# Kernel tuning notes

Hardware: AMD Instinct MI355X
Metric: run time of the kernel (lower is better)

## Reference

```python
import jax, jax.numpy as jnp
import numpy as np

B, T, HID = 4, 2048, 2048
H, DK, DV = 16, 128, 128
EPS = 1e-5


def setup_inputs() -> dict:
    key = jax.random.key(0)
    ks = jax.random.split(key, 14)
    w = lambda k, shape, s=0.02: jax.random.normal(k, shape, jnp.float32) * s
    return dict(
        hidden_states=jax.random.normal(ks[0], (B, T, HID), jnp.float32),
        recurrent_state=jnp.zeros((B, H, DK, DV), jnp.float32),
        q_w=w(ks[1], (H * DK, HID)),
        k_w=w(ks[2], (H * DK, HID)),
        v_w=w(ks[3], (H * DV, HID)),
        f_w0=w(ks[4], (DV, HID)),
        f_w1=w(ks[5], (H * DK, DV)),
        b_w=w(ks[6], (H, HID)),
        A_log=jnp.log(jax.random.uniform(ks[7], (H,), jnp.float32, 1.0, 16.0)),
        dt_bias=w(ks[8], (H * DK,), 0.1),
        g_w0=w(ks[9], (DV, HID)),
        g_w1=w(ks[10], (H * DV, DV)),
        g_b1=w(ks[11], (H * DV,), 0.1),
        o_norm_weight=jnp.ones((DV,), jnp.float32),
        o_w=w(ks[12], (HID, H * DV)),
    )


def _l2norm(x):
    return x * jax.lax.rsqrt(jnp.sum(x * x, -1, keepdims=True) + 1e-6)


def _kda_scan(q, k, v, g, beta, S0):
    # time-major inputs: q,k,g [T,B,H,DK]; v [T,B,H,DV]; beta [T,B,H]; S0 [B,H,DK,DV]
    scale = DK ** -0.5

    def step(S, inp):
        qt, kt, vt, gt, bt = inp
        S = S * jnp.exp(gt)[..., None]                      # per-key-dim decay
        kv = jnp.einsum('bhk,bhkv->bhv', kt, S)             # current readout for k
        delta = (vt - kv) * bt[..., None]                   # beta-weighted correction
        S = S + kt[..., :, None] * delta[..., None, :]      # rank-1 delta update
        ot = jnp.einsum('bhk,bhkv->bhv', qt * scale, S)
        return S, ot

    S, o = jax.lax.scan(step, S0, (q, k, v, g, beta))
    return o, S


def reference(hidden_states, recurrent_state, q_w, k_w, v_w, f_w0, f_w1, b_w,
              A_log, dt_bias, g_w0, g_w1, g_b1, o_norm_weight, o_w):
    h = hidden_states
    q = jax.nn.silu(h @ q_w.T).reshape(B, T, H, DK)
    k = jax.nn.silu(h @ k_w.T).reshape(B, T, H, DK)
    v = jax.nn.silu(h @ v_w.T).reshape(B, T, H, DV)
    # fused_kda_gate: g = -exp(A_log) * softplus(g + dt_bias), per key channel
    g = ((h @ f_w0.T) @ f_w1.T).reshape(B, T, H, DK)
    g = -jnp.exp(A_log)[None, None, :, None] * jax.nn.softplus(g + dt_bias.reshape(H, DK))
    beta = jax.nn.sigmoid(h @ b_w.T)  # [B,T,H]
    q = _l2norm(q)
    k = _l2norm(k)
    tm = lambda x: jnp.swapaxes(x, 0, 1)  # -> time-major
    o, S = _kda_scan(tm(q), tm(k), tm(v), tm(g), tm(beta), recurrent_state)
    o = jnp.swapaxes(o, 0, 1)  # [B,T,H,DV]
    factor = ((h @ g_w0.T) @ g_w1.T + g_b1).reshape(B, T, H, DV)
    # FusedRMSNormGated(activation='sigmoid'): rmsnorm then sigmoid gate
    o = o * jax.lax.rsqrt(jnp.mean(o * o, -1, keepdims=True) + EPS)
    o = o * o_norm_weight * jax.nn.sigmoid(factor)
    out = o.reshape(B, T, H * DV) @ o_w.T
    return out, S
```

## Files before the change

kernel.cpp:

```cpp
#include <hip/hip_runtime.h>
#include <math.h>


typedef short short8 __attribute__((ext_vector_type(8)));
typedef float f32x4 __attribute__((ext_vector_type(4)));
typedef unsigned short ushort_t;

enum { M_PLAIN = 0, M_QKV = 1, M_LOWRANK = 2, M_GATE = 3, M_FACTOR = 4 };

__device__ __forceinline__ unsigned short f32_to_bf16(float f) {
  unsigned int u = __float_as_uint(f);
  u += 0x7FFFu + ((u >> 16) & 1u);
  return (unsigned short)(u >> 16);
}

__device__ __forceinline__ float silu(float x) { return x / (1.f + __expf(-x)); }

__device__ __forceinline__ void gld_lds16(const void* g, void* l) {
  __builtin_amdgcn_global_load_lds(
      (const __attribute__((address_space(1))) unsigned int*)g,
      (__attribute__((address_space(3))) unsigned int*)l, 16, 0, 0);
}

__device__ __forceinline__ float row16_sum(float x) {
  x += __int_as_float(__builtin_amdgcn_update_dpp(0, __float_as_int(x), 0xB1, 0xF, 0xF, true));
  x += __int_as_float(__builtin_amdgcn_update_dpp(0, __float_as_int(x), 0x4E, 0xF, 0xF, true));
  x += __int_as_float(__builtin_amdgcn_update_dpp(0, __float_as_int(x), 0x141, 0xF, 0xF, true));
  x += __int_as_float(__builtin_amdgcn_update_dpp(0, __float_as_int(x), 0x140, 0xF, 0xF, true));
  return x;
}

__global__ __launch_bounds__(256) void gemm_bf16(
    const ushort_t* __restrict__ A, const ushort_t* __restrict__ W,
    int M, int N, int K, int mode,
    float* __restrict__ f0, float* __restrict__ f1, float* __restrict__ f2,
    ushort_t* __restrict__ b0, ushort_t* __restrict__ b1,
    const float* __restrict__ bias, const float* __restrict__ A_log,
    const float* __restrict__ dt_bias) {
  __shared__ alignas(16) ushort_t As[4096];
  __shared__ alignas(16) ushort_t Bs[4096];
  __shared__ float l2s[2][128];
  const int tid = threadIdx.x;
  const int wv = tid >> 6, ln = tid & 63;
  const int bm = blockIdx.y * 128, bn = blockIdx.x * 128;
  const int wm = wv >> 1, wn = wv & 1;

  const int srow = tid >> 2;
  const int skg = (tid & 3) ^ ((srow >> 1) & 3);
  const size_t ag0 = (size_t)(bm + srow) * K + skg * 8;
  const size_t ag1 = ag0 + (size_t)64 * K;
  const size_t bg0 = (size_t)(bn + srow) * K + skg * 8;
  const size_t bg1 = bg0 + (size_t)64 * K;
  char* const lA = (char*)As;
  char* const lB = (char*)Bs;
  const int wbase = wv * 1024;

  const int fr = ln & 15, fq = ln >> 4;
  const int pg = fq ^ ((fr >> 1) & 3);
  int aoff[4], boff[4];
#pragma unroll
  for (int i = 0; i < 4; i++) {
    aoff[i] = (wm * 64 + i * 16 + fr) * 64 + pg * 16;
    boff[i] = (wn * 64 + i * 16 + fr) * 64 + pg * 16;
  }

  f32x4 acc[4][4];
#pragma unroll
  for (int i = 0; i < 4; i++)
#pragma unroll
    for (int j = 0; j < 4; j++) {
      acc[i][j][0] = 0.f; acc[i][j][1] = 0.f; acc[i][j][2] = 0.f; acc[i][j][3] = 0.f;
    }

  for (int k0 = 0; k0 < K; k0 += 32) {
    gld_lds16(A + ag0 + k0, lA + wbase);
    gld_lds16(A + ag1 + k0, lA + 4096 + wbase);
    gld_lds16(W + bg0 + k0, lB + wbase);
    gld_lds16(W + bg1 + k0, lB + 4096 + wbase);
    __syncthreads();
    short8 af[4], bf[4];
#pragma unroll
    for (int i = 0; i < 4; i++) af[i] = *(const short8*)(lA + aoff[i]);
#pragma unroll
    for (int i = 0; i < 4; i++) bf[i] = *(const short8*)(lB + boff[i]);
#pragma unroll
    for (int i = 0; i < 4; i++)
#pragma unroll
      for (int j = 0; j < 4; j++)
        acc[i][j] = __builtin_amdgcn_mfma_f32_16x16x32_bf16(af[i], bf[j], acc[i][j], 0, 0, 0);
    __syncthreads();
  }

  const int cc = ln & 15, cq = ln >> 4;

  if (mode == M_QKV) {
#pragma unroll
    for (int i = 0; i < 4; i++)
#pragma unroll
      for (int j = 0; j < 4; j++)
#pragma unroll
        for (int r = 0; r < 4; r++) acc[i][j][r] = silu(acc[i][j][r]);
    const bool isqk = (bn < 4096);
    float invr[4][4];
    if (isqk) {
      const float scale = (bn < 2048) ? 0.08838834764831845f : 1.0f;
#pragma unroll
      for (int i = 0; i < 4; i++)
#pragma unroll
        for (int r = 0; r < 4; r++) {
          float ss = 0.f;
#pragma unroll
          for (int j = 0; j < 4; j++) ss = fmaf(acc[i][j][r], acc[i][j][r], ss);
          ss = row16_sum(ss);
          if (cc == 0) l2s[wn][wm * 64 + i * 16 + cq * 4 + r] = ss;
        }
      __syncthreads();
#pragma unroll
      for (int i = 0; i < 4; i++)
#pragma unroll
        for (int r = 0; r < 4; r++) {
          const int rl = wm * 64 + i * 16 + cq * 4 + r;
          invr[i][r] = rsqrtf(l2s[0][rl] + l2s[1][rl] + 1e-6f) * scale;
        }
    } else {
#pragma unroll
      for (int i = 0; i < 4; i++)
#pragma unroll
        for (int r = 0; r < 4; r++) invr[i][r] = 1.f;
    }
    float* dst = (bn < 2048) ? f0 : ((bn < 4096) ? f1 : f2);
    const int nb = bn & 2047;
#pragma unroll
    for (int i = 0; i < 4; i++)
#pragma unroll
      for (int r = 0; r < 4; r++) {
        const int gm = bm + wm * 64 + i * 16 + cq * 4 + r;
#pragma unroll
        for (int j = 0; j < 4; j++) {
          const int gn = nb + wn * 64 + j * 16 + cc;
          dst[(size_t)gm * 2048 + gn] = acc[i][j][r] * invr[i][r];
        }
      }
    return;
  }

  if (mode == M_LOWRANK) {
#pragma unroll
    for (int i = 0; i < 4; i++)
#pragma unroll
      for (int r = 0; r < 4; r++) {
        const int gm = bm + wm * 64 + i * 16 + cq * 4 + r;
#pragma unroll
        for (int j = 0; j < 4; j++) {
          const int gn = bn + wn * 64 + j * 16 + cc;
          const float x = acc[i][j][r];
          if (gn < 128) b0[(size_t)gm * 128 + gn] = f32_to_bf16(x);
          else if (gn < 256) b1[(size_t)gm * 128 + (gn - 128)] = f32_to_bf16(x);
          else if (gn < 272) f0[(size_t)gm * 16 + (gn - 256)] = 1.f / (1.f + __expf(-x));
        }
      }
    return;
  }

#pragma unroll
  for (int i = 0; i < 4; i++)
#pragma unroll
    for (int r = 0; r < 4; r++) {
      const int gm = bm + wm * 64 + i * 16 + cq * 4 + r;
#pragma unroll
      for (int j = 0; j < 4; j++) {
        const int gn = bn + wn * 64 + j * 16 + cc;
        float x = acc[i][j][r];
        if (mode == M_FACTOR) x += bias[gn];
        else if (mode == M_GATE) {
          const float y = x + dt_bias[gn];
          const float sp = fmaxf(y, 0.f) + log1pf(__expf(-fabsf(y)));
          x = __expf(-__expf(A_log[gn >> 7]) * sp);
        }
        f0[(size_t)gm * N + gn] = x;
      }
    }
}

__global__ __launch_bounds__(256) void cast_bf16(const float* __restrict__ x,
                                                 ushort_t* __restrict__ y, int n) {
  const int i = (blockIdx.x * 256 + threadIdx.x) * 4;
  if (i >= n) return;
  const float4 v = *(const float4*)&x[i];
  union { ushort_t u[4]; uint2 v2; } o;
  o.u[0] = f32_to_bf16(v.x); o.u[1] = f32_to_bf16(v.y);
  o.u[2] = f32_to_bf16(v.z); o.u[3] = f32_to_bf16(v.w);
  *(uint2*)&y[i] = o.v2;
}

__global__ __launch_bounds__(64, 2) void kda_scan(
    const float* __restrict__ q, const float* __restrict__ k,
    const float* __restrict__ v, const float* __restrict__ ge,
    const float* __restrict__ beta, const float* __restrict__ S0,
    float* __restrict__ o, float* __restrict__ S_out) {
  const int bid = blockIdx.x;
  const int bh = (((bid >> 3) & 7) << 3) | (bid & 7);
  const int cg = bid >> 6;
  const int h = bh & 15, b = bh >> 4;
  const int ln = threadIdx.x;
  const int cl = ln >> 4, kg = ln & 15;
  const int col = cg * 4 + cl;
  const int kof = kg * 8;

  __shared__ alignas(16) char lds[12288];

  const size_t s_base = (size_t)bh * (128 * 128);
  const size_t rb = (size_t)b * (2048 * 2048) + (size_t)h * 128;
  const size_t bbase = (size_t)(b * 2048) * 16 + h;

  const char* kc = (const char*)(k + rb);
  const char* qc = (const char*)(q + rb);
  const char* gc = (const char*)(ge + rb);
  const float* vbp  = v + rb;
  const float* vbp2 = vbp + 2048;
  const float* bbp  = beta + bbase;
  const float* bbp2 = bbp + 16;
  float* obp  = o + rb;
  float* obp2 = obp + 2048;
  const float* S0b = S0 + s_base;

  const int cpos = ln & 31;
  const int gch = (cpos & ~1) | ((cpos & 1) ^ ((cpos >> 3) & 1));
  const unsigned lane_src = (unsigned)((ln >> 5) * 8192 + gch * 16);

  const unsigned rd0 = (unsigned)(kg * 32 + ((0 ^ ((kg >> 2) & 1)) * 16));
  const unsigned rd1 = (unsigned)(kg * 32 + ((1 ^ ((kg >> 2) & 1)) * 16));

  const unsigned voff_v = (unsigned)(col * 4);
  const unsigned voff_b = 0u;
  const unsigned voff_o = (unsigned)(col * 4);

  float S[8];
#pragma unroll
  for (int j = 0; j < 8; ++j) {
    const unsigned offs = (unsigned)(((kof + j) * 128 + col) * 4);
    asm volatile("global_load_dword %0, %1, %2" : "=v"(S[j]) : "v"(offs), "s"(S0b));
  }

  float Vs[8], Bs[8], Os[8];
  f32x4 K0a, K1a, Q0a, Q1a, G0a, G1a;
  f32x4 K0b, K1b, Q0b, Q1b, G0b, G1b;

#define WAITV(N) do { asm volatile("s_waitcnt vmcnt(" #N ")" ::: "memory"); \
                      __builtin_amdgcn_sched_barrier(0); } while (0)
#define WAITL(N) do { asm volatile("s_waitcnt lgkmcnt(" #N ")" ::: "memory"); \
                      __builtin_amdgcn_sched_barrier(0); } while (0)
#define DSR(dst, a, IMM) \
  asm volatile("ds_read_b128 %0, %1 offset:%c2" : "=v"(dst) : "v"(a), "n"(IMM))

#define READS(SFX, SL, PH)                                    \
  do {                                                        \
    DSR(K0##SFX, rd0, ((SL)*3 + 0) * 1024 + (PH)*512);        \
    DSR(K1##SFX, rd1, ((SL)*3 + 0) * 1024 + (PH)*512);        \
    DSR(Q0##SFX, rd0, ((SL)*3 + 1) * 1024 + (PH)*512);        \
    DSR(Q1##SFX, rd1, ((SL)*3 + 1) * 1024 + (PH)*512);        \
    DSR(G0##SFX, rd0, ((SL)*3 + 2) * 1024 + (PH)*512);        \
    DSR(G1##SFX, rd1, ((SL)*3 + 2) * 1024 + (PH)*512);        \
  } while (0)

#define STAGE(SL)                                                                                    \
  do {                                                                                               \
    gld_lds16(kc + lane_src, lds + ((SL)*3 + 0) * 1024); kc += 16384;                                \
    gld_lds16(qc + lane_src, lds + ((SL)*3 + 1) * 1024); qc += 16384;                                \
    gld_lds16(gc + lane_src, lds + ((SL)*3 + 2) * 1024); gc += 16384;                                \
    asm volatile("global_load_dword %0, %1, %2" : "=v"(Vs[2*(SL)])   : "v"(voff_v), "s"(vbp));       \
    asm volatile("global_load_dword %0, %1, %2" : "=v"(Vs[2*(SL)+1]) : "v"(voff_v), "s"(vbp2));      \
    vbp += 4096; vbp2 += 4096;                                                                       \
    asm volatile("global_load_dword %0, %1, %2" : "=v"(Bs[2*(SL)])   : "v"(voff_b), "s"(bbp));       \
    asm volatile("global_load_dword %0, %1, %2" : "=v"(Bs[2*(SL)+1]) : "v"(voff_b), "s"(bbp2));      \
    bbp += 32; bbp2 += 32;                                                                           \
  } while (0)

#define STORES(U)                                                                                    \
  do {                                                                                               \
    if (kg == 0) {                                                                                   \
      asm volatile("global_store_dword %0, %1, %2" :: "v"(voff_o), "v"(Os[(U)-1]), "s"(obp) : "memory");  \
      asm volatile("global_store_dword %0, %1, %2" :: "v"(voff_o), "v"(Os[(U)]), "s"(obp2) : "memory");   \
    }                                                                                                \
    obp += 4096; obp2 += 4096;                                                                       \
  } while (0)

#define COMPUTE(SFX, U)                                                                              \
  do {                                                                                               \
    float p0 = 0.f, p1 = 0.f, o0 = 0.f, o1 = 0.f, d0 = 0.f, d1 = 0.f;                                \
    S[0] *= G0##SFX[0]; p0 = fmaf(K0##SFX[0], S[0], p0); o0 = fmaf(Q0##SFX[0], S[0], o0); d0 = fmaf(Q0##SFX[0], K0##SFX[0], d0); \
    S[1] *= G0##SFX[1]; p1 = fmaf(K0##SFX[1], S[1], p1); o1 = fmaf(Q0##SFX[1], S[1], o1); d1 = fmaf(Q0##SFX[1], K0##SFX[1], d1); \
    S[2] *= G0##SFX[2]; p0 = fmaf(K0##SFX[2], S[2], p0); o0 = fmaf(Q0##SFX[2], S[2], o0); d0 = fmaf(Q0##SFX[2], K0##SFX[2], d0); \
    S[3] *= G0##SFX[3]; p1 = fmaf(K0##SFX[3], S[3], p1); o1 = fmaf(Q0##SFX[3], S[3], o1); d1 = fmaf(Q0##SFX[3], K0##SFX[3], d1); \
    S[4] *= G1##SFX[0]; p0 = fmaf(K1##SFX[0], S[4], p0); o0 = fmaf(Q1##SFX[0], S[4], o0); d0 = fmaf(Q1##SFX[0], K1##SFX[0], d0); \
    S[5] *= G1##SFX[1]; p1 = fmaf(K1##SFX[1], S[5], p1); o1 = fmaf(Q1##SFX[1], S[5], o1); d1 = fmaf(Q1##SFX[1], K1##SFX[1], d1); \
    S[6] *= G1##SFX[2]; p0 = fmaf(K1##SFX[2], S[6], p0); o0 = fmaf(Q1##SFX[2], S[6], o0); d0 = fmaf(Q1##SFX[2], K1##SFX[2], d0); \
    S[7] *= G1##SFX[3]; p1 = fmaf(K1##SFX[3], S[7], p1); o1 = fmaf(Q1##SFX[3], S[7], o1); d1 = fmaf(Q1##SFX[3], K1##SFX[3], d1); \
    const float p  = row16_sum(p0 + p1);                                                             \
    const float oq = row16_sum(o0 + o1);                                                             \
    const float qk = row16_sum(d0 + d1);                                                             \
    const float delta = (Vs[(U)] - p) * Bs[(U)];                                                     \
    Os[(U)] = fmaf(qk, delta, oq);                                                                   \
    S[0] = fmaf(K0##SFX[0], delta, S[0]);                                                            \
    S[1] = fmaf(K0##SFX[1], delta, S[1]);                                                            \
    S[2] = fmaf(K0##SFX[2], delta, S[2]);                                                            \
    S[3] = fmaf(K0##SFX[3], delta, S[3]);                                                            \
    S[4] = fmaf(K1##SFX[0], delta, S[4]);                                                            \
    S[5] = fmaf(K1##SFX[1], delta, S[5]);                                                            \
    S[6] = fmaf(K1##SFX[2], delta, S[6]);                                                            \
    S[7] = fmaf(K1##SFX[3], delta, S[7]);                                                            \
  } while (0)

#define STEP_EVEN(U, SL) \
  do { READS(b, SL, 1); WAITL(6); COMPUTE(a, U); } while (0)
#define STEP_ODD(U, SL, NSL, WV) \
  do { WAITV(WV); READS(a, NSL, 0); WAITL(6); COMPUTE(b, U); STAGE(SL); STORES(U); } while (0)

#define ITER(W1, W3, W5, W7)                          \
  do {                                                \
    STEP_EVEN(0, 0);                                  \
    STEP_ODD(1, 0, 1, W1);                            \
    STEP_EVEN(2, 1);                                  \
    STEP_ODD(3, 1, 2, W3);                            \
    STEP_EVEN(4, 2);                                  \
    STEP_ODD(5, 2, 3, W5);                            \
    STEP_EVEN(6, 3);                                  \
    STEP_ODD(7, 3, 0, W7);                            \
  } while (0)

  STAGE(0);
  STAGE(1);
  STAGE(2);
  STAGE(3);
  WAITV(21);
  READS(a, 0, 0);

  ITER(14, 16, 18, 20);
  for (int it = 1; it < 256; ++it) {
    ITER(20, 20, 20, 20);
  }

  WAITL(0);
  WAITV(0);

#pragma unroll
  for (int j = 0; j < 8; ++j)
    S_out[s_base + (size_t)(kof + j) * 128 + col] = S[j];

#undef ITER
#undef STEP_ODD
#undef STEP_EVEN
#undef COMPUTE
#undef STORES
#undef STAGE
#undef READS
#undef DSR
#undef WAITL
#undef WAITV
}

__global__ __launch_bounds__(256) void gate_rmsnorm(
    const float* __restrict__ o, const float* __restrict__ factor,
    const float* __restrict__ w, ushort_t* __restrict__ out) {
  const int ln = threadIdx.x & 63, wv = threadIdx.x >> 6;
  const float w0 = w[ln * 2], w1 = w[ln * 2 + 1];
  const size_t row0 = (size_t)blockIdx.x * 64 + wv * 16;
  for (int it = 0; it < 16; it++) {
    const size_t base = (row0 + it) * 128 + ln * 2;
    const float2 x = *(const float2*)&o[base];
    const float2 f = *(const float2*)&factor[base];
    float ss = fmaf(x.x, x.x, x.y * x.y);
    ss = row16_sum(ss);
    ss += __shfl_xor(ss, 16);
    ss += __shfl_xor(ss, 32);
    const float r = rsqrtf(ss * (1.f / 128.f) + 1e-5f);
    const float y0 = x.x * r * w0 / (1.f + __expf(-f.x));
    const float y1 = x.y * r * w1 / (1.f + __expf(-f.y));
    *(unsigned int*)&out[base] =
        (unsigned int)f32_to_bf16(y0) | ((unsigned int)f32_to_bf16(y1) << 16);
  }
}

extern "C" void kernel_launch(void* const* d_in, const int* in_sizes, int n_in,
                              void* d_out, int out_size, void* d_ws, size_t ws_size,
                              hipStream_t stream) {
  const float* h    = (const float*)d_in[0];
  const float* S0   = (const float*)d_in[1];
  const float* q_w  = (const float*)d_in[2];
  const float* k_w  = (const float*)d_in[3];
  const float* v_w  = (const float*)d_in[4];
  const float* f_w0 = (const float*)d_in[5];
  const float* f_w1 = (const float*)d_in[6];
  const float* b_w  = (const float*)d_in[7];
  const float* A_log  = (const float*)d_in[8];
  const float* dt_b   = (const float*)d_in[9];
  const float* g_w0 = (const float*)d_in[10];
  const float* g_w1 = (const float*)d_in[11];
  const float* g_b1 = (const float*)d_in[12];
  const float* o_nw = (const float*)d_in[13];
  const float* o_w  = (const float*)d_in[14];

  float* outp = (float*)d_out;
  float* Sout = outp + (size_t)8192 * 2048;

  const size_t BIG = (size_t)8192 * 2048;
  float* ws = (float*)d_ws;
  float* vbuf  = ws;
  float* qbuf  = vbuf + BIG;
  float* kbuf  = qbuf + BIG;
  float* betab = kbuf + BIG;
  ushort_t* fpreb = (ushort_t*)(betab + (size_t)8192 * 16);
  ushort_t* gpreb = fpreb + (size_t)8192 * 128;
  ushort_t* wf1   = gpreb + (size_t)8192 * 128;
  ushort_t* wg1   = wf1 + (size_t)2048 * 128;
  ushort_t* wo    = wg1 + (size_t)2048 * 128;
  ushort_t* wlow  = wo + (size_t)2048 * 2048;
  ushort_t* hb    = wlow + (size_t)384 * 2048;
  ushort_t* wqkv  = hb + BIG;
  float* obuf = (float*)hb;
  ushort_t* gatedb = (ushort_t*)qbuf;

  const dim3 blk(256);

  cast_bf16<<<16384, blk, 0, stream>>>(h, hb, 8192 * 2048);
  cast_bf16<<<4096, blk, 0, stream>>>(q_w, wqkv, 2048 * 2048);
  cast_bf16<<<4096, blk, 0, stream>>>(k_w, wqkv + (size_t)2048 * 2048, 2048 * 2048);
  cast_bf16<<<4096, blk, 0, stream>>>(v_w, wqkv + (size_t)4096 * 2048, 2048 * 2048);
  cast_bf16<<<4096, blk, 0, stream>>>(o_w, wo, 2048 * 2048);
  cast_bf16<<<256, blk, 0, stream>>>(f_w0, wlow, 128 * 2048);
  cast_bf16<<<256, blk, 0, stream>>>(g_w0, wlow + (size_t)128 * 2048, 128 * 2048);
  cast_bf16<<<32, blk, 0, stream>>>(b_w, wlow + (size_t)256 * 2048, 16 * 2048);
  cast_bf16<<<256, blk, 0, stream>>>(f_w1, wf1, 2048 * 128);
  cast_bf16<<<256, blk, 0, stream>>>(g_w1, wg1, 2048 * 128);

  gemm_bf16<<<dim3(48, 64), blk, 0, stream>>>(hb, wqkv, 8192, 6144, 2048, M_QKV,
      qbuf, kbuf, vbuf, nullptr, nullptr, nullptr, nullptr, nullptr);
  gemm_bf16<<<dim3(3, 64), blk, 0, stream>>>(hb, wlow, 8192, 384, 2048, M_LOWRANK,
      betab, nullptr, nullptr, fpreb, gpreb, nullptr, nullptr, nullptr);
  gemm_bf16<<<dim3(16, 64), blk, 0, stream>>>(fpreb, wf1, 8192, 2048, 128, M_GATE,
      outp, nullptr, nullptr, nullptr, nullptr, nullptr, A_log, dt_b);
  kda_scan<<<2048, 64, 0, stream>>>(qbuf, kbuf, vbuf, outp, betab, S0, obuf, Sout);
  gemm_bf16<<<dim3(16, 64), blk, 0, stream>>>(gpreb, wg1, 8192, 2048, 128, M_FACTOR,
      outp, nullptr, nullptr, nullptr, nullptr, g_b1, nullptr, nullptr);
  gate_rmsnorm<<<2048, blk, 0, stream>>>(obuf, outp, o_nw, gatedb);
  gemm_bf16<<<dim3(16, 64), blk, 0, stream>>>(gatedb, wo, 8192, 2048, 2048, M_PLAIN,
      outp, nullptr, nullptr, nullptr, nullptr, nullptr, nullptr, nullptr);
}
```

Before: 1.828 ms.

## Remap scan lanes to 32 key-groups by 2 value columns with cross-half reduction

Each lane of the KDA scan kernel now holds 4 key rows across 2 value columns, where before it held 8 key rows of 1 column. Wavefront halves split the key dimension and are combined with a permlane32 swap. This cuts the LDS reads per step from six to three and lets V, O and the state move as dwordx2. The cost is a longer reduction chain per dot product (row16 plus a cross-half swap) and five reductions instead of three, on the serial recurrence's critical path.

Measured after the change: 2.061 ms. 12.8% more time.

```diff
diff --git a/kernel.cpp b/kernel.cpp
--- a/kernel.cpp
+++ b/kernel.cpp
@@ -4,6 +4,8 @@
 
 typedef short short8 __attribute__((ext_vector_type(8)));
 typedef float f32x4 __attribute__((ext_vector_type(4)));
+typedef float f32x2 __attribute__((ext_vector_type(2)));
+typedef int int2v __attribute__((ext_vector_type(2)));
 typedef unsigned short ushort_t;
 
 enum { M_PLAIN = 0, M_QKV = 1, M_LOWRANK = 2, M_GATE = 3, M_FACTOR = 4 };
@@ -28,6 +30,13 @@
   x += __int_as_float(__builtin_amdgcn_update_dpp(0, __float_as_int(x), 0x141, 0xF, 0xF, true));
   x += __int_as_float(__builtin_amdgcn_update_dpp(0, __float_as_int(x), 0x140, 0xF, 0xF, true));
   return x;
+}
+
+__device__ __forceinline__ float sum32(float x) {
+  x = row16_sum(x);
+  int2v r = __builtin_amdgcn_permlane32_swap(__float_as_int(x), __float_as_int(x),
+                                             false, false);
+  return __int_as_float(r.x) + __int_as_float(r.y);
 }
 
 __global__ __launch_bounds__(256) void gemm_bf16(
@@ -203,9 +212,10 @@
   const int cg = bid >> 6;
   const int h = bh & 15, b = bh >> 4;
   const int ln = threadIdx.x;
-  const int cl = ln >> 4, kg = ln & 15;
-  const int col = cg * 4 + cl;
-  const int kof = kg * 8;
+  const int cl = (ln >> 4) & 1;
+  const int kg5 = (ln & 15) | (((ln >> 5) & 1) << 4);
+  const int col0 = cg * 4 + cl * 2;
+  const int k0i = kg5 * 4;
 
   __shared__ alignas(16) char lds[12288];
 
@@ -224,27 +234,24 @@
   float* obp2 = obp + 2048;
   const float* S0b = S0 + s_base;
 
-  const int cpos = ln & 31;
-  const int gch = (cpos & ~1) | ((cpos & 1) ^ ((cpos >> 3) & 1));
-  const unsigned lane_src = (unsigned)((ln >> 5) * 8192 + gch * 16);
-
-  const unsigned rd0 = (unsigned)(kg * 32 + ((0 ^ ((kg >> 2) & 1)) * 16));
-  const unsigned rd1 = (unsigned)(kg * 32 + ((1 ^ ((kg >> 2) & 1)) * 16));
-
-  const unsigned voff_v = (unsigned)(col * 4);
+  const unsigned lane_src = (unsigned)((ln >> 5) * 8192 + (ln & 31) * 16);
+  const unsigned rdK = (unsigned)(kg5 * 16);
+
+  const unsigned voff_v = (unsigned)(col0 * 4);
   const unsigned voff_b = 0u;
-  const unsigned voff_o = (unsigned)(col * 4);
-
-  float S[8];
-#pragma unroll
-  for (int j = 0; j < 8; ++j) {
-    const unsigned offs = (unsigned)(((kof + j) * 128 + col) * 4);
-    asm volatile("global_load_dword %0, %1, %2" : "=v"(S[j]) : "v"(offs), "s"(S0b));
-  }
-
-  float Vs[8], Bs[8], Os[8];
-  f32x4 K0a, K1a, Q0a, Q1a, G0a, G1a;
-  f32x4 K0b, K1b, Q0b, Q1b, G0b, G1b;
+  const unsigned voff_o = (unsigned)(col0 * 4);
+
+  f32x2 S2[4];
+#pragma unroll
+  for (int j = 0; j < 4; ++j) {
+    const unsigned offs = (unsigned)(((k0i + j) * 128 + col0) * 4);
+    asm volatile("global_load_dwordx2 %0, %1, %2" : "=v"(S2[j]) : "v"(offs), "s"(S0b));
+  }
+
+  f32x2 Vs2[8], Os2[8];
+  float Bs[8];
+  f32x4 Ka, Qa, Ga;
+  f32x4 Kb, Qb, Gb;
 
 #define WAITV(N) do { asm volatile("s_waitcnt vmcnt(" #N ")" ::: "memory"); \
                       __builtin_amdgcn_sched_barrier(0); } while (0)
@@ -255,12 +262,9 @@
 
 #define READS(SFX, SL, PH)                                    \
   do {                                                        \
-    DSR(K0##SFX, rd0, ((SL)*3 + 0) * 1024 + (PH)*512);        \
-    DSR(K1##SFX, rd1, ((SL)*3 + 0) * 1024 + (PH)*512);        \
-    DSR(Q0##SFX, rd0, ((SL)*3 + 1) * 1024 + (PH)*512);        \
-    DSR(Q1##SFX, rd1, ((SL)*3 + 1) * 1024 + (PH)*512);        \
-    DSR(G0##SFX, rd0, ((SL)*3 + 2) * 1024 + (PH)*512);        \
-    DSR(G1##SFX, rd1, ((SL)*3 + 2) * 1024 + (PH)*512);        \
+    DSR(K##SFX, rdK, ((SL)*3 + 0) * 1024 + (PH)*512);         \
+    DSR(Q##SFX, rdK, ((SL)*3 + 1) * 1024 + (PH)*512);         \
+    DSR(G##SFX, rdK, ((SL)*3 + 2) * 1024 + (PH)*512);         \
   } while (0)
 
 #define STAGE(SL)                                                                                    \
@@ -268,8 +272,8 @@
     gld_lds16(kc + lane_src, lds + ((SL)*3 + 0) * 1024); kc += 16384;                                \
     gld_lds16(qc + lane_src, lds + ((SL)*3 + 1) * 1024); qc += 16384;                                \
     gld_lds16(gc + lane_src, lds + ((SL)*3 + 2) * 1024); gc += 16384;                                \
-    asm volatile("global_load_dword %0, %1, %2" : "=v"(Vs[2*(SL)])   : "v"(voff_v), "s"(vbp));       \
-    asm volatile("global_load_dword %0, %1, %2" : "=v"(Vs[2*(SL)+1]) : "v"(voff_v), "s"(vbp2));      \
+    asm volatile("global_load_dwordx2 %0, %1, %2" : "=v"(Vs2[2*(SL)])   : "v"(voff_v), "s"(vbp));    \
+    asm volatile("global_load_dwordx2 %0, %1, %2" : "=v"(Vs2[2*(SL)+1]) : "v"(voff_v), "s"(vbp2));   \
     vbp += 4096; vbp2 += 4096;                                                                       \
     asm volatile("global_load_dword %0, %1, %2" : "=v"(Bs[2*(SL)])   : "v"(voff_b), "s"(bbp));       \
     asm volatile("global_load_dword %0, %1, %2" : "=v"(Bs[2*(SL)+1]) : "v"(voff_b), "s"(bbp2));      \
@@ -278,43 +282,45 @@
 
 #define STORES(U)                                                                                    \
   do {                                                                                               \
-    if (kg == 0) {                                                                                   \
-      asm volatile("global_store_dword %0, %1, %2" :: "v"(voff_o), "v"(Os[(U)-1]), "s"(obp) : "memory");  \
-      asm volatile("global_store_dword %0, %1, %2" :: "v"(voff_o), "v"(Os[(U)]), "s"(obp2) : "memory");   \
+    if ((ln & 47) == 0) {                                                                            \
+      asm volatile("global_store_dwordx2 %0, %1, %2" :: "v"(voff_o), "v"(Os2[(U)-1]), "s"(obp) : "memory");  \
+      asm volatile("global_store_dwordx2 %0, %1, %2" :: "v"(voff_o), "v"(Os2[(U)]), "s"(obp2) : "memory");   \
     }                                                                                                \
     obp += 4096; obp2 += 4096;                                                                       \
   } while (0)
 
-#define COMPUTE(SFX, U)                                                                              \
+#define COMPUTE(F, U)                                                                                \
   do {                                                                                               \
-    float p0 = 0.f, p1 = 0.f, o0 = 0.f, o1 = 0.f, d0 = 0.f, d1 = 0.f;                                \
-    S[0] *= G0##SFX[0]; p0 = fmaf(K0##SFX[0], S[0], p0); o0 = fmaf(Q0##SFX[0], S[0], o0); d0 = fmaf(Q0##SFX[0], K0##SFX[0], d0); \
-    S[1] *= G0##SFX[1]; p1 = fmaf(K0##SFX[1], S[1], p1); o1 = fmaf(Q0##SFX[1], S[1], o1); d1 = fmaf(Q0##SFX[1], K0##SFX[1], d1); \
-    S[2] *= G0##SFX[2]; p0 = fmaf(K0##SFX[2], S[2], p0); o0 = fmaf(Q0##SFX[2], S[2], o0); d0 = fmaf(Q0##SFX[2], K0##SFX[2], d0); \
-    S[3] *= G0##SFX[3]; p1 = fmaf(K0##SFX[3], S[3], p1); o1 = fmaf(Q0##SFX[3], S[3], o1); d1 = fmaf(Q0##SFX[3], K0##SFX[3], d1); \
-    S[4] *= G1##SFX[0]; p0 = fmaf(K1##SFX[0], S[4], p0); o0 = fmaf(Q1##SFX[0], S[4], o0); d0 = fmaf(Q1##SFX[0], K1##SFX[0], d0); \
-    S[5] *= G1##SFX[1]; p1 = fmaf(K1##SFX[1], S[5], p1); o1 = fmaf(Q1##SFX[1], S[5], o1); d1 = fmaf(Q1##SFX[1], K1##SFX[1], d1); \
-    S[6] *= G1##SFX[2]; p0 = fmaf(K1##SFX[2], S[6], p0); o0 = fmaf(Q1##SFX[2], S[6], o0); d0 = fmaf(Q1##SFX[2], K1##SFX[2], d0); \
-    S[7] *= G1##SFX[3]; p1 = fmaf(K1##SFX[3], S[7], p1); o1 = fmaf(Q1##SFX[3], S[7], o1); d1 = fmaf(Q1##SFX[3], K1##SFX[3], d1); \
-    const float p  = row16_sum(p0 + p1);                                                             \
-    const float oq = row16_sum(o0 + o1);                                                             \
-    const float qk = row16_sum(d0 + d1);                                                             \
-    const float delta = (Vs[(U)] - p) * Bs[(U)];                                                     \
-    Os[(U)] = fmaf(qk, delta, oq);                                                                   \
-    S[0] = fmaf(K0##SFX[0], delta, S[0]);                                                            \
-    S[1] = fmaf(K0##SFX[1], delta, S[1]);                                                            \
-    S[2] = fmaf(K0##SFX[2], delta, S[2]);                                                            \
-    S[3] = fmaf(K0##SFX[3], delta, S[3]);                                                            \
-    S[4] = fmaf(K1##SFX[0], delta, S[4]);                                                            \
-    S[5] = fmaf(K1##SFX[1], delta, S[5]);                                                            \
-    S[6] = fmaf(K1##SFX[2], delta, S[6]);                                                            \
-    S[7] = fmaf(K1##SFX[3], delta, S[7]);                                                            \
+    S2[0] *= G##F[0]; S2[1] *= G##F[1]; S2[2] *= G##F[2]; S2[3] *= G##F[3];                          \
+    float p0 = K##F[0] * S2[0].x;  float p1 = K##F[0] * S2[0].y;                                     \
+    float o0 = Q##F[0] * S2[0].x;  float o1 = Q##F[0] * S2[0].y;                                     \
+    float d  = Q##F[0] * K##F[0];                                                                    \
+    p0 = fmaf(K##F[1], S2[1].x, p0); p1 = fmaf(K##F[1], S2[1].y, p1);                                \
+    o0 = fmaf(Q##F[1], S2[1].x, o0); o1 = fmaf(Q##F[1], S2[1].y, o1);                                \
+    d  = fmaf(Q##F[1], K##F[1], d);                                                                  \
+    p0 = fmaf(K##F[2], S2[2].x, p0); p1 = fmaf(K##F[2], S2[2].y, p1);                                \
+    o0 = fmaf(Q##F[2], S2[2].x, o0); o1 = fmaf(Q##F[2], S2[2].y, o1);                                \
+    d  = fmaf(Q##F[2], K##F[2], d);                                                                  \
+    p0 = fmaf(K##F[3], S2[3].x, p0); p1 = fmaf(K##F[3], S2[3].y, p1);                                \
+    o0 = fmaf(Q##F[3], S2[3].x, o0); o1 = fmaf(Q##F[3], S2[3].y, o1);                                \
+    d  = fmaf(Q##F[3], K##F[3], d);                                                                  \
+    p0 = sum32(p0); p1 = sum32(p1);                                                                  \
+    o0 = sum32(o0); o1 = sum32(o1);                                                                  \
+    d  = sum32(d);                                                                                   \
+    const float dl0 = (Vs2[(U)].x - p0) * Bs[(U)];                                                   \
+    const float dl1 = (Vs2[(U)].y - p1) * Bs[(U)];                                                   \
+    Os2[(U)].x = fmaf(d, dl0, o0);                                                                   \
+    Os2[(U)].y = fmaf(d, dl1, o1);                                                                   \
+    S2[0].x = fmaf(K##F[0], dl0, S2[0].x); S2[0].y = fmaf(K##F[0], dl1, S2[0].y);                    \
+    S2[1].x = fmaf(K##F[1], dl0, S2[1].x); S2[1].y = fmaf(K##F[1], dl1, S2[1].y);                    \
+    S2[2].x = fmaf(K##F[2], dl0, S2[2].x); S2[2].y = fmaf(K##F[2], dl1, S2[2].y);                    \
+    S2[3].x = fmaf(K##F[3], dl0, S2[3].x); S2[3].y = fmaf(K##F[3], dl1, S2[3].y);                    \
   } while (0)
 
 #define STEP_EVEN(U, SL) \
-  do { READS(b, SL, 1); WAITL(6); COMPUTE(a, U); } while (0)
+  do { READS(b, SL, 1); WAITL(3); COMPUTE(a, U); } while (0)
 #define STEP_ODD(U, SL, NSL, WV) \
-  do { WAITV(WV); READS(a, NSL, 0); WAITL(6); COMPUTE(b, U); STAGE(SL); STORES(U); } while (0)
+  do { WAITV(WV); READS(a, NSL, 0); WAITL(3); COMPUTE(b, U); STAGE(SL); STORES(U); } while (0)
 
 #define ITER(W1, W3, W5, W7)                          \
   do {                                                \
@@ -344,8 +350,8 @@
   WAITV(0);
 
 #pragma unroll
-  for (int j = 0; j < 8; ++j)
-    S_out[s_base + (size_t)(kof + j) * 128 + col] = S[j];
+  for (int j = 0; j < 4; ++j)
+    *(f32x2*)&S_out[s_base + (size_t)(k0i + j) * 128 + col0] = S2[j];
 
 #undef ITER
 #undef STEP_ODD
```

## Store q and k in bf16 and restage scan pipeline four timesteps per slot

Applied to the files above, without the earlier changes.

The QKV GEMM epilogue now writes normalized q and k as bf16 instead of fp32, and the recurrent scan kernel reads them as bf16, unpacking them with shifts and masks. The scan's LDS staging is reorganized so each slot holds four timesteps of k/q/g, with wait counts and the V/beta/O load and store patterns adjusted to match. This halves the global and LDS traffic for q and k in the bandwidth- and latency-bound sequential scan. In exchange it adds bf16 rounding error on q and k that feeds a long recurrence, and it makes the hand-tuned wait counts more intricate.

New measurement: 1.742 ms. 1.05x faster.

```diff
diff --git a/kernel.cpp b/kernel.cpp
--- a/kernel.cpp
+++ b/kernel.cpp
@@ -4,6 +4,7 @@
 
 typedef short short8 __attribute__((ext_vector_type(8)));
 typedef float f32x4 __attribute__((ext_vector_type(4)));
+typedef int int4v __attribute__((ext_vector_type(4)));
 typedef unsigned short ushort_t;
 
 enum { M_PLAIN = 0, M_QKV = 1, M_LOWRANK = 2, M_GATE = 3, M_FACTOR = 4 };
@@ -128,7 +129,6 @@
 #pragma unroll
         for (int r = 0; r < 4; r++) invr[i][r] = 1.f;
     }
-    float* dst = (bn < 2048) ? f0 : ((bn < 4096) ? f1 : f2);
     const int nb = bn & 2047;
 #pragma unroll
     for (int i = 0; i < 4; i++)
@@ -138,7 +138,13 @@
 #pragma unroll
         for (int j = 0; j < 4; j++) {
           const int gn = nb + wn * 64 + j * 16 + cc;
-          dst[(size_t)gm * 2048 + gn] = acc[i][j][r] * invr[i][r];
+          const float val = acc[i][j][r] * invr[i][r];
+          if (bn < 4096) {
+            ushort_t* db = (bn < 2048) ? b0 : b1;
+            db[(size_t)gm * 2048 + gn] = f32_to_bf16(val);
+          } else {
+            f2[(size_t)gm * 2048 + gn] = val;
+          }
         }
       }
     return;
@@ -194,7 +200,7 @@
 }
 
 __global__ __launch_bounds__(64, 2) void kda_scan(
-    const float* __restrict__ q, const float* __restrict__ k,
+    const ushort_t* __restrict__ q, const ushort_t* __restrict__ k,
     const float* __restrict__ v, const float* __restrict__ ge,
     const float* __restrict__ beta, const float* __restrict__ S0,
     float* __restrict__ o, float* __restrict__ S_out) {
@@ -207,33 +213,34 @@
   const int col = cg * 4 + cl;
   const int kof = kg * 8;
 
-  __shared__ alignas(16) char lds[12288];
+  __shared__ alignas(16) char lds[16384];
 
   const size_t s_base = (size_t)bh * (128 * 128);
   const size_t rb = (size_t)b * (2048 * 2048) + (size_t)h * 128;
   const size_t bbase = (size_t)(b * 2048) * 16 + h;
 
-  const char* kc = (const char*)(k + rb);
-  const char* qc = (const char*)(q + rb);
-  const char* gc = (const char*)(ge + rb);
-  const float* vbp  = v + rb;
-  const float* vbp2 = vbp + 2048;
-  const float* bbp  = beta + bbase;
-  const float* bbp2 = bbp + 16;
-  float* obp  = o + rb;
-  float* obp2 = obp + 2048;
+  const char* kc = (const char*)k + rb * 2;
+  const char* qc = (const char*)q + rb * 2;
+  const char* gc = (const char*)ge + rb * 4;
+  const float* vbp = v + rb;
+  const float* bbp = beta + bbase;
+  float* obp = o + rb;
   const float* S0b = S0 + s_base;
 
+  const unsigned lane_src_kq = (unsigned)((ln >> 4) * 4096 + (ln & 15) * 16);
   const int cpos = ln & 31;
   const int gch = (cpos & ~1) | ((cpos & 1) ^ ((cpos >> 3) & 1));
-  const unsigned lane_src = (unsigned)((ln >> 5) * 8192 + gch * 16);
-
-  const unsigned rd0 = (unsigned)(kg * 32 + ((0 ^ ((kg >> 2) & 1)) * 16));
-  const unsigned rd1 = (unsigned)(kg * 32 + ((1 ^ ((kg >> 2) & 1)) * 16));
-
-  const unsigned voff_v = (unsigned)(col * 4);
+  const unsigned lane_src_g = (unsigned)((ln >> 5) * 8192 + gch * 16);
+
+  const unsigned rdK = (unsigned)(kg * 16);
+  const unsigned rd0g = (unsigned)(kg * 32 + ((0 ^ ((kg >> 2) & 1)) * 16));
+  const unsigned rd1g = (unsigned)(kg * 32 + ((1 ^ ((kg >> 2) & 1)) * 16));
+
+  const unsigned voff_v0 = (unsigned)(col * 4);
+  const unsigned voff_v1 = voff_v0 + 8192u;
+  const unsigned voff_v2 = voff_v0 + 16384u;
+  const unsigned voff_v3 = voff_v0 + 24576u;
   const unsigned voff_b = 0u;
-  const unsigned voff_o = (unsigned)(col * 4);
 
   float S[8];
 #pragma unroll
@@ -242,9 +249,9 @@
     asm volatile("global_load_dword %0, %1, %2" : "=v"(S[j]) : "v"(offs), "s"(S0b));
   }
 
-  float Vs[8], Bs[8], Os[8];
-  f32x4 K0a, K1a, Q0a, Q1a, G0a, G1a;
-  f32x4 K0b, K1b, Q0b, Q1b, G0b, G1b;
+  float Vs[4][4], Bs[4][4], Os[4];
+  int4v Kda, Qda, Kdb, Qdb;
+  f32x4 G0a, G1a, G0b, G1b;
 
 #define WAITV(N) do { asm volatile("s_waitcnt vmcnt(" #N ")" ::: "memory"); \
                       __builtin_amdgcn_sched_barrier(0); } while (0)
@@ -255,89 +262,103 @@
 
 #define READS(SFX, SL, PH)                                    \
   do {                                                        \
-    DSR(K0##SFX, rd0, ((SL)*3 + 0) * 1024 + (PH)*512);        \
-    DSR(K1##SFX, rd1, ((SL)*3 + 0) * 1024 + (PH)*512);        \
-    DSR(Q0##SFX, rd0, ((SL)*3 + 1) * 1024 + (PH)*512);        \
-    DSR(Q1##SFX, rd1, ((SL)*3 + 1) * 1024 + (PH)*512);        \
-    DSR(G0##SFX, rd0, ((SL)*3 + 2) * 1024 + (PH)*512);        \
-    DSR(G1##SFX, rd1, ((SL)*3 + 2) * 1024 + (PH)*512);        \
-  } while (0)
-
-#define STAGE(SL)                                                                                    \
+    DSR(Kd##SFX, rdK,  (SL)*4096 + (PH)*256);                 \
+    DSR(Qd##SFX, rdK,  (SL)*4096 + 1024 + (PH)*256);          \
+    DSR(G0##SFX, rd0g, (SL)*4096 + 2048 + (PH)*512);          \
+    DSR(G1##SFX, rd1g, (SL)*4096 + 2048 + (PH)*512);          \
+  } while (0)
+
+#define RESTAGE(SL)                                                                                  \
   do {                                                                                               \
-    gld_lds16(kc + lane_src, lds + ((SL)*3 + 0) * 1024); kc += 16384;                                \
-    gld_lds16(qc + lane_src, lds + ((SL)*3 + 1) * 1024); qc += 16384;                                \
-    gld_lds16(gc + lane_src, lds + ((SL)*3 + 2) * 1024); gc += 16384;                                \
-    asm volatile("global_load_dword %0, %1, %2" : "=v"(Vs[2*(SL)])   : "v"(voff_v), "s"(vbp));       \
-    asm volatile("global_load_dword %0, %1, %2" : "=v"(Vs[2*(SL)+1]) : "v"(voff_v), "s"(vbp2));      \
-    vbp += 4096; vbp2 += 4096;                                                                       \
-    asm volatile("global_load_dword %0, %1, %2" : "=v"(Bs[2*(SL)])   : "v"(voff_b), "s"(bbp));       \
-    asm volatile("global_load_dword %0, %1, %2" : "=v"(Bs[2*(SL)+1]) : "v"(voff_b), "s"(bbp2));      \
-    bbp += 32; bbp2 += 32;                                                                           \
-  } while (0)
-
-#define STORES(U)                                                                                    \
+    gld_lds16(kc + lane_src_kq, lds + (SL)*4096);          kc += 16384;                              \
+    gld_lds16(qc + lane_src_kq, lds + (SL)*4096 + 1024);   qc += 16384;                              \
+    gld_lds16(gc + lane_src_g,  lds + (SL)*4096 + 2048);                                             \
+    gld_lds16(gc + 16384 + lane_src_g, lds + (SL)*4096 + 3072); gc += 32768;                         \
+    asm volatile("global_load_dword %0, %1, %2" : "=v"(Vs[SL][0]) : "v"(voff_v0), "s"(vbp));         \
+    asm volatile("global_load_dword %0, %1, %2" : "=v"(Vs[SL][1]) : "v"(voff_v1), "s"(vbp));         \
+    asm volatile("global_load_dword %0, %1, %2" : "=v"(Vs[SL][2]) : "v"(voff_v2), "s"(vbp));         \
+    asm volatile("global_load_dword %0, %1, %2" : "=v"(Vs[SL][3]) : "v"(voff_v3), "s"(vbp));         \
+    vbp += 8192;                                                                                     \
+    asm volatile("global_load_dword %0, %1, %2"            : "=v"(Bs[SL][0]) : "v"(voff_b), "s"(bbp)); \
+    asm volatile("global_load_dword %0, %1, %2 offset:64"  : "=v"(Bs[SL][1]) : "v"(voff_b), "s"(bbp)); \
+    asm volatile("global_load_dword %0, %1, %2 offset:128" : "=v"(Bs[SL][2]) : "v"(voff_b), "s"(bbp)); \
+    asm volatile("global_load_dword %0, %1, %2 offset:192" : "=v"(Bs[SL][3]) : "v"(voff_b), "s"(bbp)); \
+    bbp += 64;                                                                                       \
+  } while (0)
+
+#define STORES(SL)                                                                                   \
   do {                                                                                               \
     if (kg == 0) {                                                                                   \
-      asm volatile("global_store_dword %0, %1, %2" :: "v"(voff_o), "v"(Os[(U)-1]), "s"(obp) : "memory");  \
-      asm volatile("global_store_dword %0, %1, %2" :: "v"(voff_o), "v"(Os[(U)]), "s"(obp2) : "memory");   \
+      asm volatile("global_store_dword %0, %1, %2" :: "v"(voff_v0), "v"(Os[0]), "s"(obp) : "memory"); \
+      asm volatile("global_store_dword %0, %1, %2" :: "v"(voff_v1), "v"(Os[1]), "s"(obp) : "memory"); \
+      asm volatile("global_store_dword %0, %1, %2" :: "v"(voff_v2), "v"(Os[2]), "s"(obp) : "memory"); \
+      asm volatile("global_store_dword %0, %1, %2" :: "v"(voff_v3), "v"(Os[3]), "s"(obp) : "memory"); \
     }                                                                                                \
-    obp += 4096; obp2 += 4096;                                                                       \
-  } while (0)
-
-#define COMPUTE(SFX, U)                                                                              \
+    obp += 8192;                                                                                     \
+  } while (0)
+
+#define COMPUTE(F, SS, U)                                                                            \
   do {                                                                                               \
+    const int4v kd = Kd##F; const int4v qd = Qd##F;                                                  \
+    const float k0 = __int_as_float(kd[0] << 16), k1 = __int_as_float(kd[0] & 0xffff0000);           \
+    const float k2 = __int_as_float(kd[1] << 16), k3 = __int_as_float(kd[1] & 0xffff0000);           \
+    const float k4 = __int_as_float(kd[2] << 16), k5 = __int_as_float(kd[2] & 0xffff0000);           \
+    const float k6 = __int_as_float(kd[3] << 16), k7 = __int_as_float(kd[3] & 0xffff0000);           \
+    const float q0 = __int_as_float(qd[0] << 16), q1 = __int_as_float(qd[0] & 0xffff0000);           \
+    const float q2 = __int_as_float(qd[1] << 16), q3 = __int_as_float(qd[1] & 0xffff0000);           \
+    const float q4 = __int_as_float(qd[2] << 16), q5 = __int_as_float(qd[2] & 0xffff0000);           \
+    const float q6 = __int_as_float(qd[3] << 16), q7 = __int_as_float(qd[3] & 0xffff0000);           \
     float p0 = 0.f, p1 = 0.f, o0 = 0.f, o1 = 0.f, d0 = 0.f, d1 = 0.f;                                \
-    S[0] *= G0##SFX[0]; p0 = fmaf(K0##SFX[0], S[0], p0); o0 = fmaf(Q0##SFX[0], S[0], o0); d0 = fmaf(Q0##SFX[0], K0##SFX[0], d0); \
-    S[1] *= G0##SFX[1]; p1 = fmaf(K0##SFX[1], S[1], p1); o1 = fmaf(Q0##SFX[1], S[1], o1); d1 = fmaf(Q0##SFX[1], K0##SFX[1], d1); \
-    S[2] *= G0##SFX[2]; p0 = fmaf(K0##SFX[2], S[2], p0); o0 = fmaf(Q0##SFX[2], S[2], o0); d0 = fmaf(Q0##SFX[2], K0##SFX[2], d0); \
-    S[3] *= G0##SFX[3]; p1 = fmaf(K0##SFX[3], S[3], p1); o1 = fmaf(Q0##SFX[3], S[3], o1); d1 = fmaf(Q0##SFX[3], K0##SFX[3], d1); \
-    S[4] *= G1##SFX[0]; p0 = fmaf(K1##SFX[0], S[4], p0); o0 = fmaf(Q1##SFX[0], S[4], o0); d0 = fmaf(Q1##SFX[0], K1##SFX[0], d0); \
-    S[5] *= G1##SFX[1]; p1 = fmaf(K1##SFX[1], S[5], p1); o1 = fmaf(Q1##SFX[1], S[5], o1); d1 = fmaf(Q1##SFX[1], K1##SFX[1], d1); \
-    S[6] *= G1##SFX[2]; p0 = fmaf(K1##SFX[2], S[6], p0); o0 = fmaf(Q1##SFX[2], S[6], o0); d0 = fmaf(Q1##SFX[2], K1##SFX[2], d0); \
-    S[7] *= G1##SFX[3]; p1 = fmaf(K1##SFX[3], S[7], p1); o1 = fmaf(Q1##SFX[3], S[7], o1); d1 = fmaf(Q1##SFX[3], K1##SFX[3], d1); \
+    S[0] *= G0##F[0]; p0 = fmaf(k0, S[0], p0); o0 = fmaf(q0, S[0], o0); d0 = fmaf(q0, k0, d0);       \
+    S[1] *= G0##F[1]; p1 = fmaf(k1, S[1], p1); o1 = fmaf(q1, S[1], o1); d1 = fmaf(q1, k1, d1);       \
+    S[2] *= G0##F[2]; p0 = fmaf(k2, S[2], p0); o0 = fmaf(q2, S[2], o0); d0 = fmaf(q2, k2, d0);       \
+    S[3] *= G0##F[3]; p1 = fmaf(k3, S[3], p1); o1 = fmaf(q3, S[3], o1); d1 = fmaf(q3, k3, d1);       \
+    S[4] *= G1##F[0]; p0 = fmaf(k4, S[4], p0); o0 = fmaf(q4, S[4], o0); d0 = fmaf(q4, k4, d0);       \
+    S[5] *= G1##F[1]; p1 = fmaf(k5, S[5], p1); o1 = fmaf(q5, S[5], o1); d1 = fmaf(q5, k5, d1);       \
+    S[6] *= G1##F[2]; p0 = fmaf(k6, S[6], p0); o0 = fmaf(q6, S[6], o0); d0 = fmaf(q6, k6, d0);       \
+    S[7] *= G1##F[3]; p1 = fmaf(k7, S[7], p1); o1 = fmaf(q7, S[7], o1); d1 = fmaf(q7, k7, d1);       \
     const float p  = row16_sum(p0 + p1);                                                             \
     const float oq = row16_sum(o0 + o1);                                                             \
     const float qk = row16_sum(d0 + d1);                                                             \
-    const float delta = (Vs[(U)] - p) * Bs[(U)];                                                     \
-    Os[(U)] = fmaf(qk, delta, oq);                                                                   \
-    S[0] = fmaf(K0##SFX[0], delta, S[0]);                                                            \
-    S[1] = fmaf(K0##SFX[1], delta, S[1]);                                                            \
-    S[2] = fmaf(K0##SFX[2], delta, S[2]);                                                            \
-    S[3] = fmaf(K0##SFX[3], delta, S[3]);                                                            \
-    S[4] = fmaf(K1##SFX[0], delta, S[4]);                                                            \
-    S[5] = fmaf(K1##SFX[1], delta, S[5]);                                                            \
-    S[6] = fmaf(K1##SFX[2], delta, S[6]);                                                            \
-    S[7] = fmaf(K1##SFX[3], delta, S[7]);                                                            \
-  } while (0)
-
-#define STEP_EVEN(U, SL) \
-  do { READS(b, SL, 1); WAITL(6); COMPUTE(a, U); } while (0)
-#define STEP_ODD(U, SL, NSL, WV) \
-  do { WAITV(WV); READS(a, NSL, 0); WAITL(6); COMPUTE(b, U); STAGE(SL); STORES(U); } while (0)
-
-#define ITER(W1, W3, W5, W7)                          \
+    const float delta = (Vs[SS][U] - p) * Bs[SS][U];                                                 \
+    Os[U] = fmaf(qk, delta, oq);                                                                     \
+    S[0] = fmaf(k0, delta, S[0]);                                                                    \
+    S[1] = fmaf(k1, delta, S[1]);                                                                    \
+    S[2] = fmaf(k2, delta, S[2]);                                                                    \
+    S[3] = fmaf(k3, delta, S[3]);                                                                    \
+    S[4] = fmaf(k4, delta, S[4]);                                                                    \
+    S[5] = fmaf(k5, delta, S[5]);                                                                    \
+    S[6] = fmaf(k6, delta, S[6]);                                                                    \
+    S[7] = fmaf(k7, delta, S[7]);                                                                    \
+  } while (0)
+
+#define SLOT(SL, NS, WV)                                           \
+  do {                                                             \
+    READS(b, SL, 1); WAITL(4); COMPUTE(a, SL, 0);                  \
+    READS(a, SL, 2); WAITL(4); COMPUTE(b, SL, 1);                  \
+    READS(b, SL, 3); WAITL(4); COMPUTE(a, SL, 2);                  \
+    WAITV(WV); READS(a, NS, 0); WAITL(4); COMPUTE(b, SL, 3);       \
+    RESTAGE(SL); STORES(SL);                                       \
+  } while (0)
+
+#define ITER(W0, W1, W2, W3)                          \
   do {                                                \
-    STEP_EVEN(0, 0);                                  \
-    STEP_ODD(1, 0, 1, W1);                            \
-    STEP_EVEN(2, 1);                                  \
-    STEP_ODD(3, 1, 2, W3);                            \
-    STEP_EVEN(4, 2);                                  \
-    STEP_ODD(5, 2, 3, W5);                            \
-    STEP_EVEN(6, 3);                                  \
-    STEP_ODD(7, 3, 0, W7);                            \
-  } while (0)
-
-  STAGE(0);
-  STAGE(1);
-  STAGE(2);
-  STAGE(3);
-  WAITV(21);
+    SLOT(0, 1, W0);                                   \
+    SLOT(1, 2, W1);                                   \
+    SLOT(2, 3, W2);                                   \
+    SLOT(3, 0, W3);                                   \
+  } while (0)
+
+  RESTAGE(0);
+  RESTAGE(1);
+  RESTAGE(2);
+  RESTAGE(3);
+  WAITV(36);
   READS(a, 0, 0);
 
-  ITER(14, 16, 18, 20);
-  for (int it = 1; it < 256; ++it) {
-    ITER(20, 20, 20, 20);
+  ITER(24, 28, 32, 36);
+  for (int it = 1; it < 128; ++it) {
+    ITER(36, 36, 36, 36);
   }
 
   WAITL(0);
@@ -348,11 +369,10 @@
     S_out[s_base + (size_t)(kof + j) * 128 + col] = S[j];
 
 #undef ITER
-#undef STEP_ODD
-#undef STEP_EVEN
+#undef SLOT
 #undef COMPUTE
 #undef STORES
-#undef STAGE
+#undef RESTAGE
 #undef READS
 #undef DSR
 #undef WAITL
@@ -419,6 +439,8 @@
   ushort_t* wqkv  = hb + BIG;
   float* obuf = (float*)hb;
   ushort_t* gatedb = (ushort_t*)qbuf;
+  ushort_t* qb16 = (ushort_t*)qbuf;
+  ushort_t* kb16 = (ushort_t*)kbuf;
 
   const dim3 blk(256);
 
@@ -434,12 +456,12 @@
   cast_bf16<<<256, blk, 0, stream>>>(g_w1, wg1, 2048 * 128);
 
   gemm_bf16<<<dim3(48, 64), blk, 0, stream>>>(hb, wqkv, 8192, 6144, 2048, M_QKV,
-      qbuf, kbuf, vbuf, nullptr, nullptr, nullptr, nullptr, nullptr);
+      nullptr, nullptr, vbuf, qb16, kb16, nullptr, nullptr, nullptr);
   gemm_bf16<<<dim3(3, 64), blk, 0, stream>>>(hb, wlow, 8192, 384, 2048, M_LOWRANK,
       betab, nullptr, nullptr, fpreb, gpreb, nullptr, nullptr, nullptr);
   gemm_bf16<<<dim3(16, 64), blk, 0, stream>>>(fpreb, wf1, 8192, 2048, 128, M_GATE,
       outp, nullptr, nullptr, nullptr, nullptr, nullptr, A_log, dt_b);
-  kda_scan<<<2048, 64, 0, stream>>>(qbuf, kbuf, vbuf, outp, betab, S0, obuf, Sout);
+  kda_scan<<<2048, 64, 0, stream>>>(qb16, kb16, vbuf, outp, betab, S0, obuf, Sout);
   gemm_bf16<<<dim3(16, 64), blk, 0, stream>>>(gpreb, wg1, 8192, 2048, 128, M_FACTOR,
       outp, nullptr, nullptr, nullptr, nullptr, g_b1, nullptr, nullptr);
   gate_rmsnorm<<<2048, blk, 0, stream>>>(obuf, outp, o_nw, gatedb);
```
